# Optimization experiments

Hardware: AMD Instinct MI355X
Metric: run time of the kernel (lower is better)

## Reference

```python
import jax, jax.numpy as jnp
import numpy as np

C = 1.0      # base manifold curvature (Lorentz c)
C_E = 1.0    # expert manifold curvature (all experts init to c=1.0)
K = 1        # n_activated_experts (top-k)
SCALE = 2.0  # LResNet scale for shared-expert combine
EPS = 1e-8


def _lorentz_swiglu(x, W1, W3, W2, c_mid, c_out, prescale):
    """LorentzExpert / LorentzFeedForward: SwiGLU on space coords with Lorentz time lift.
    x: [T, D] (full Lorentz vector). W1,W3: [I-1, D]; W2: [D-1, I]. Returns [T, D]."""
    if prescale:
        x = x * np.float32(np.sqrt(C_E / C))  # x * sqrt(c_expert / c)
    s1 = jax.nn.silu(x @ W1.T)                 # [T, I-1] w1(x, return_space=True)
    s3 = x @ W3.T                              # [T, I-1] w3(x, return_space=True)
    sp = s1 * s3                               # gated space part
    t = jnp.sqrt(jnp.clip((sp * sp).sum(-1, keepdims=True) + c_mid, EPS))
    h = jnp.concatenate([t, sp], axis=-1)      # [T, I] point on expert manifold
    o = h @ W2.T                               # [T, D-1] w2 space output
    ot = jnp.sqrt(jnp.clip((o * o).sum(-1, keepdims=True) + c_out, EPS))
    return jnp.concatenate([ot, o], axis=-1)   # [T, D] on base manifold


def setup_inputs() -> dict:
    key = jax.random.key(0)
    ks = jax.random.split(key, 9)
    T, D, E, I = 2048, 1024, 8, 1024
    x = jax.random.normal(ks[0], (T, D), jnp.float32)
    gate_w = jax.random.normal(ks[1], (E, D - 1), jnp.float32) / np.sqrt(D - 1)
    gate_b = jax.random.normal(ks[2], (E,), jnp.float32) * 0.01
    W1 = jax.random.normal(ks[3], (E, I - 1, D), jnp.float32) / np.sqrt(D)
    W3 = jax.random.normal(ks[4], (E, I - 1, D), jnp.float32) / np.sqrt(D)
    W2 = jax.random.normal(ks[5], (E, D - 1, I), jnp.float32) / np.sqrt(I)
    Ws1 = jax.random.normal(ks[6], (I - 1, D), jnp.float32) / np.sqrt(D)
    Ws3 = jax.random.normal(ks[7], (I - 1, D), jnp.float32) / np.sqrt(D)
    Ws2 = jax.random.normal(ks[8], (D - 1, I), jnp.float32) / np.sqrt(I)
    return {"x": x, "gate_w": gate_w, "gate_b": gate_b, "W1": W1, "W3": W3,
            "W2": W2, "Ws1": Ws1, "Ws3": Ws3, "Ws2": Ws2}


def reference(x, gate_w, gate_b, W1, W3, W2, Ws1, Ws3, Ws2):
    T, D = x.shape
    E = gate_w.shape[0]
    # ---- Gate (softmax scoring, n_groups == 1, route_scale == 1.0) ----
    logits = x[:, 1:] @ gate_w.T                                    # [T, E]
    scores = jax.nn.softmax(logits.astype(jnp.float32), axis=-1)
    biased = scores + gate_b                                        # bias only affects routing
    _, idx = jax.lax.top_k(biased, K)                               # [T, K]
    weights = jnp.take_along_axis(scores, idx, axis=-1).astype(x.dtype)  # [T, K]
    # dense per-token expert gate weights [T, E]
    oh = jax.nn.one_hot(idx, E, dtype=x.dtype)                      # [T, K, E]
    gw = (oh * weights[..., None]).sum(axis=1)                      # [T, E]
    # ---- y init: project(zeros) -> [sqrt(c), 0, ..., 0] ----
    y0 = jnp.concatenate([jnp.full((T, 1), np.sqrt(C), x.dtype),
                          jnp.zeros((T, D - 1), x.dtype)], axis=-1)
    # ---- routed experts (dense reference: every expert on every token, masked combine) ----
    e_out = jax.vmap(lambda w1, w3, w2: _lorentz_swiglu(x, w1, w3, w2, C_E, C, True))(W1, W3, W2)  # [E, T, D]
    y = y0 + jnp.einsum('te,etd->td', gw, e_out)
    # ---- shared expert (LorentzFeedForward, stays on base manifold) ----
    z = _lorentz_swiglu(x, Ws1, Ws3, Ws2, C, C, False)
    # ---- LResNet weighted sum: normalize (z + scale*y) back to manifold ----
    comb = z + SCALE * y
    li = (comb[:, 1:] ** 2).sum(-1, keepdims=True) - comb[:, :1] ** 2  # Lorentz inner <comb,comb>
    out = np.float32(np.sqrt(C)) * comb / jnp.sqrt(jnp.clip(jnp.abs(li), EPS))
    return out
```

## Files before the change

### kernel.cpp

```cpp
#include <hip/hip_runtime.h>

typedef __bf16 bf16;
typedef __attribute__((ext_vector_type(8))) __bf16 bf16x8;
typedef __attribute__((ext_vector_type(4))) float floatx4;

#define TOK 2048
#define DD  1024
#define NE  8
#define SMAX 24

#define MFMA16(A,B,C) __builtin_amdgcn_mfma_f32_16x16x32_bf16(A,B,C,0,0,0)

__device__ __forceinline__ void load_lds16(const bf16* g, bf16* l) {
  __builtin_amdgcn_global_load_lds(
      (const __attribute__((address_space(1))) void*)g,
      (__attribute__((address_space(3))) void*)l, 16, 0, 0);
}

#define WBAR(N) asm volatile("s_waitcnt vmcnt(" #N ")\n\ts_barrier" ::: "memory")
#define BARO    asm volatile("s_barrier" ::: "memory")

#define NCVT (8*2046 + 2046 + 8*1023 + 1023)
#define GATEB TOK
__global__ __launch_bounds__(256) void prep_kernel(
    const float* __restrict__ x, const float* __restrict__ gate_w,
    const float* __restrict__ gate_b,
    const float* __restrict__ W1, const float* __restrict__ W3,
    const float* __restrict__ W2, const float* __restrict__ Ws1,
    const float* __restrict__ Ws3, const float* __restrict__ Ws2,
    bf16* __restrict__ x_bf, int* __restrict__ eidx, float* __restrict__ ewgt,
    float* __restrict__ ss,
    bf16* __restrict__ w13, bf16* __restrict__ ws13,
    bf16* __restrict__ w2b, bf16* __restrict__ ws2b,
    float* __restrict__ w2c0_r, float* __restrict__ w2c0_s,
    bf16* __restrict__ h_r, bf16* __restrict__ h_s)
{
  const int bid = blockIdx.x, tid = threadIdx.x;

  if (bid >= GATEB) {
    const int r = bid - GATEB;
    const float* src; bf16* dst;
    float* c0dst = nullptr;
    if (r < 8 * 2046) {
      const int e = r / 2046, q = r % 2046;
      src = ((q & 1) ? W3 : W1) + ((size_t)e * 1023 + (q >> 1)) * 1024;
      dst = w13 + (size_t)r * 1024;
    } else if (r < 8 * 2046 + 2046) {
      const int q = r - 8 * 2046;
      src = ((q & 1) ? Ws3 : Ws1) + (size_t)(q >> 1) * 1024;
      dst = ws13 + (size_t)q * 1024;
    } else if (r < 8 * 2046 + 2046 + 8 * 1023) {
      const int q = r - (8 * 2046 + 2046);
      src = W2 + (size_t)q * 1024;
      dst = w2b + (size_t)q * 1024;
      c0dst = w2c0_r + (size_t)(q / 1023) * 1024 + (q % 1023);
    } else {
      const int q = r - (8 * 2046 + 2046 + 8 * 1023);
      src = Ws2 + (size_t)q * 1024;
      dst = ws2b + (size_t)q * 1024;
      c0dst = w2c0_s + q;
    }
    const float4 f = ((const float4*)src)[tid];
    if (tid == 0 && c0dst) *c0dst = f.x;
    union { bf16 h[4]; uint2 u; } p;
    p.h[0] = (bf16)f.x; p.h[1] = (bf16)f.y; p.h[2] = (bf16)f.z; p.h[3] = (bf16)f.w;
    ((uint2*)dst)[tid] = p.u;
    return;
  }

  const int t = bid;
  if (tid < 2) ss[tid * TOK + t] = 0.f;
  if (tid == 2) h_r[(size_t)t * 1024] = (bf16)0.f;
  if (tid == 3) h_s[(size_t)t * 1024] = (bf16)0.f;
  const float4 v = ((const float4*)(x + (size_t)t * DD))[tid];
  union { bf16 h[4]; uint2 u; } pk;
  pk.h[0] = (bf16)v.x; pk.h[1] = (bf16)v.y; pk.h[2] = (bf16)v.z; pk.h[3] = (bf16)v.w;
  ((uint2*)(x_bf + (size_t)t * DD))[tid] = pk.u;

  float acc[NE];
#pragma unroll
  for (int e = 0; e < NE; ++e) acc[e] = 0.f;
  const float vv[4] = {v.x, v.y, v.z, v.w};
#pragma unroll
  for (int i = 0; i < 4; ++i) {
    const int d = tid * 4 + i;
    if (d >= 1) {
#pragma unroll
      for (int e = 0; e < NE; ++e) acc[e] += vv[i] * gate_w[e * (DD - 1) + d - 1];
    }
  }
#pragma unroll
  for (int off = 32; off > 0; off >>= 1) {
#pragma unroll
    for (int e = 0; e < NE; ++e) acc[e] += __shfl_down(acc[e], off);
  }
  __shared__ float red[4][NE];
  const int wid = tid >> 6, lane = tid & 63;
  if (lane == 0) {
#pragma unroll
    for (int e = 0; e < NE; ++e) red[wid][e] = acc[e];
  }
  __syncthreads();
  if (tid == 0) {
    float lg[NE];
#pragma unroll
    for (int e = 0; e < NE; ++e) lg[e] = red[0][e] + red[1][e] + red[2][e] + red[3][e];
    float m = lg[0];
    for (int e = 1; e < NE; ++e) m = fmaxf(m, lg[e]);
    float ex[NE], s = 0.f;
    for (int e = 0; e < NE; ++e) { ex[e] = expf(lg[e] - m); s += ex[e]; }
    const float inv = 1.f / s;
    int best = 0; float bb = ex[0] * inv + gate_b[0];
    for (int e = 1; e < NE; ++e) {
      const float b = ex[e] * inv + gate_b[e];
      if (b > bb) { bb = b; best = e; }
    }
    eidx[t] = best;
    ewgt[t] = ex[best] * inv;
  }
}

__global__ __launch_bounds__(256) void route_kernel(
    const int* __restrict__ eidx, int* __restrict__ perm,
    int* __restrict__ pos_of, int4* __restrict__ wl, int* __restrict__ n1)
{
  __shared__ int cnt[NE], off[NE], bas[NE + 1];
  const int tid = threadIdx.x;
  if (tid < NE) cnt[tid] = 0;
  __syncthreads();
  for (int t = tid; t < TOK; t += 256) atomicAdd(&cnt[eidx[t]], 1);
  __syncthreads();
  if (tid == 0) {
    int run = 0;
    for (int e = 0; e < NE; ++e) { bas[e] = run; off[e] = run; run += cnt[e]; }
    bas[NE] = run;
    int n = 0;
    for (int e = 0; e < NE; ++e)
      for (int r0 = 0; r0 < cnt[e]; r0 += 256) {
        int rows = cnt[e] - r0; if (rows > 256) rows = 256;
        wl[n++] = make_int4(bas[e] + r0, rows, e, 0);
      }
    for (int r0 = 0; r0 < TOK; r0 += 256) wl[n++] = make_int4(r0, 256, NE, 0);
    *n1 = n;
  }
  __syncthreads();
  for (int t = tid; t < TOK; t += 256) {
    const int e = eidx[t];
    const int p = atomicAdd(&off[e], 1);
    perm[p] = t;
    pos_of[t] = p;
  }
}

__global__ __launch_bounds__(1024) void mlp1_kernel(
    const bf16* __restrict__ x_bf, const bf16* __restrict__ w13,
    const bf16* __restrict__ ws13,
    const int* __restrict__ perm, const int4* __restrict__ wl,
    const int* __restrict__ wl_n,
    bf16* __restrict__ h_r, bf16* __restrict__ h_s,
    float* __restrict__ ss_r, float* __restrict__ ss_z)
{
  const int bid = blockIdx.x;
  const int slot = bid % SMAX, nt = bid / SMAX;
  if (slot >= *wl_n) return;
  const int4 wle = wl[slot];
  const int mbase = wle.x, rows = wle.y, eid = wle.z;
  const int tid = threadIdx.x;
  const bool routed = (eid < NE);
  const bf16* bmat = routed ? w13 + (size_t)eid * 2046 * 1024 : ws13;
  bf16* hbuf  = routed ? h_r : h_s;
  float* ssbuf = routed ? ss_r : ss_z;

  extern __shared__ __align__(16) bf16 smem[];
  bf16* const Asb[2] = {smem, smem + 16384};
  bf16* const Bsb[2] = {smem + 32768, smem + 49152};
  __shared__ int toks[256];
  if (tid < 256) {
    int r = tid < rows ? tid : rows - 1;
    toks[tid] = routed ? perm[mbase + r] : (mbase + r);
  }
  __syncthreads();

  const int wid = tid >> 6, lane = tid & 63;
  const int srow = lane >> 3;
  const int kbg  = (lane & 7) ^ (srow & 7);
  const bf16 *aG0, *aG1, *bG0, *bG1;
  int aL0o, aL1o, bL0o, bL1o;
  {
    const int r0 = wid * 16;
    aG0 = x_bf + (size_t)toks[r0 + 0 + srow] * 1024 + kbg * 8;
    aG1 = x_bf + (size_t)toks[r0 + 8 + srow] * 1024 + kbg * 8;
    aL0o = (r0 + 0) * 64; aL1o = (r0 + 8) * 64;
    int b0 = nt * 256 + r0 + 0 + srow; if (b0 > 2045) b0 = 2045;
    int b1 = nt * 256 + r0 + 8 + srow; if (b1 > 2045) b1 = 2045;
    bG0 = bmat + (size_t)b0 * 1024 + kbg * 8;
    bG1 = bmat + (size_t)b1 * 1024 + kbg * 8;
    bL0o = (r0 + 0) * 64; bL1o = (r0 + 8) * 64;
  }

  const int lrow = lane & 15, quad = lane >> 4, sw = lane & 7;
  const int wrow = (wid >> 2) * 64, wcol = (wid & 3) * 64;
  int aoff[4], boff[4], koff[2];
#pragma unroll
  for (int mi = 0; mi < 4; ++mi) aoff[mi] = (wrow + mi * 16 + lrow) * 64;
#pragma unroll
  for (int ni = 0; ni < 4; ++ni) boff[ni] = (wcol + ni * 16 + lrow) * 64;
#pragma unroll
  for (int kk = 0; kk < 2; ++kk) koff[kk] = ((kk * 4 + quad) ^ sw) * 8;

  const floatx4 fz = {0.f, 0.f, 0.f, 0.f};
  floatx4 acc[4][4];
#pragma unroll
  for (int mi = 0; mi < 4; ++mi)
#pragma unroll
    for (int ni = 0; ni < 4; ++ni) acc[mi][ni] = fz;

#define STAGE1(KE, BUF) { \
    load_lds16(aG0 + (KE), Asb[BUF] + aL0o); load_lds16(aG1 + (KE), Asb[BUF] + aL1o); \
    load_lds16(bG0 + (KE), Bsb[BUF] + bL0o); load_lds16(bG1 + (KE), Bsb[BUF] + bL1o); }

#define COMP1(BUF) { \
_Pragma("unroll") \
    for (int kk = 0; kk < 2; ++kk) { \
      bf16x8 av[4], bv[4]; \
_Pragma("unroll") \
      for (int mi = 0; mi < 4; ++mi) av[mi] = *(const bf16x8*)(Asb[BUF] + aoff[mi] + koff[kk]); \
_Pragma("unroll") \
      for (int ni = 0; ni < 4; ++ni) bv[ni] = *(const bf16x8*)(Bsb[BUF] + boff[ni] + koff[kk]); \
_Pragma("unroll") \
      for (int mi = 0; mi < 4; ++mi) \
_Pragma("unroll") \
        for (int ni = 0; ni < 4; ++ni) \
          acc[mi][ni] = MFMA16(av[mi], bv[ni], acc[mi][ni]); \
    } }

  STAGE1(0, 0)
  STAGE1(64, 1)
#pragma unroll 1
  for (int t = 0; t < 7; ++t) {
    const int ke = t * 128;
    WBAR(4); COMP1(0) BARO; STAGE1(ke + 128, 0)
    WBAR(4); COMP1(1) BARO; STAGE1(ke + 192, 1)
  }
  WBAR(4); COMP1(0)
  WBAR(0); COMP1(1)
#undef STAGE1
#undef COMP1

#pragma unroll
  for (int mi = 0; mi < 4; ++mi) {
#pragma unroll
    for (int r = 0; r < 4; ++r) {
      const int row = wrow + mi * 16 + quad * 4 + r;
      const bool rowok = row < rows;
      float ssum = 0.f;
#pragma unroll
      for (int ni = 0; ni < 4; ++ni) {
        const float c = acc[mi][ni][r];
        const float partner = __shfl_xor(c, 1);
        const float s1 = (lane & 1) ? partner : c;
        const float s3 = (lane & 1) ? c : partner;
        const float sp = (s1 / (1.f + __expf(-s1))) * s3;
        const int P = (nt * 256 + wcol + ni * 16 + lrow) >> 1;
        const bool ok = rowok && ((lane & 1) == 0) && (P < 1023);
        if (ok) hbuf[(size_t)(mbase + row) * 1024 + 1 + P] = (bf16)sp;
        ssum += ok ? sp * sp : 0.f;
      }
      ssum += __shfl_xor(ssum, 1);
      ssum += __shfl_xor(ssum, 2);
      ssum += __shfl_xor(ssum, 4);
      ssum += __shfl_xor(ssum, 8);
      if (lrow == 0 && rowok) atomicAdd(ssbuf + mbase + row, ssum);
    }
  }
}

__global__ __launch_bounds__(1024) void mlp2_kernel(
    const bf16* __restrict__ h_r, const bf16* __restrict__ h_s,
    const bf16* __restrict__ w2b, const bf16* __restrict__ ws2b,
    const int4* __restrict__ wl, const int* __restrict__ wl_n,
    float* __restrict__ o_r0, float* __restrict__ o_r1,
    float* __restrict__ o_s0, float* __restrict__ o_s1)
{
  const int bid = blockIdx.x;
  const int slot = bid % SMAX;
  const int rest = bid / SMAX;
  const int nt = rest & 3, kh = rest >> 2;
  if (slot >= *wl_n) return;
  const int4 wle = wl[slot];
  const int mbase = wle.x, rows = wle.y, eid = wle.z;
  const int tid = threadIdx.x;
  const bool routed = (eid < NE);
  const bf16* abuf = routed ? h_r : h_s;
  const bf16* bmat = routed ? w2b + (size_t)eid * 1023 * 1024 : ws2b;
  float* obuf = routed ? (kh ? o_r1 : o_r0) : (kh ? o_s1 : o_s0);
  const int n0 = nt * 256;
  const int kbase = kh * 512;

  extern __shared__ __align__(16) bf16 smem[];
  bf16* const Asb[2] = {smem, smem + 16384};
  bf16* const Bsb[2] = {smem + 32768, smem + 49152};

  const int wid = tid >> 6, lane = tid & 63;
  const int srow = lane >> 3;
  const int kbg  = (lane & 7) ^ (srow & 7);
  const bf16 *aG0, *aG1, *bG0, *bG1;
  int aL0o, aL1o, bL0o, bL1o;
  {
    const int r0 = wid * 16;
    int ra0 = r0 + 0 + srow; if (ra0 >= rows) ra0 = rows - 1;
    int ra1 = r0 + 8 + srow; if (ra1 >= rows) ra1 = rows - 1;
    aG0 = abuf + (size_t)(mbase + ra0) * 1024 + kbase + kbg * 8;
    aG1 = abuf + (size_t)(mbase + ra1) * 1024 + kbase + kbg * 8;
    aL0o = (r0 + 0) * 64; aL1o = (r0 + 8) * 64;
    int b0 = n0 + r0 + 0 + srow; if (b0 > 1022) b0 = 1022;
    int b1 = n0 + r0 + 8 + srow; if (b1 > 1022) b1 = 1022;
    bG0 = bmat + (size_t)b0 * 1024 + kbase + kbg * 8;
    bG1 = bmat + (size_t)b1 * 1024 + kbase + kbg * 8;
    bL0o = (r0 + 0) * 64; bL1o = (r0 + 8) * 64;
  }

  const int lrow = lane & 15, quad = lane >> 4, sw = lane & 7;
  const int wrow = (wid >> 2) * 64, wcol = (wid & 3) * 64;
  int aoff[4], boff[4], koff[2];
#pragma unroll
  for (int mi = 0; mi < 4; ++mi) aoff[mi] = (wrow + mi * 16 + lrow) * 64;
#pragma unroll
  for (int ni = 0; ni < 4; ++ni) boff[ni] = (wcol + ni * 16 + lrow) * 64;
#pragma unroll
  for (int kk = 0; kk < 2; ++kk) koff[kk] = ((kk * 4 + quad) ^ sw) * 8;

  const floatx4 fz = {0.f, 0.f, 0.f, 0.f};
  floatx4 acc[4][4];
#pragma unroll
  for (int mi = 0; mi < 4; ++mi)
#pragma unroll
    for (int ni = 0; ni < 4; ++ni) acc[mi][ni] = fz;

#define STAGE2(KE, BUF) { \
    load_lds16(aG0 + (KE), Asb[BUF] + aL0o); load_lds16(aG1 + (KE), Asb[BUF] + aL1o); \
    load_lds16(bG0 + (KE), Bsb[BUF] + bL0o); load_lds16(bG1 + (KE), Bsb[BUF] + bL1o); }

#define COMP2(BUF) { \
_Pragma("unroll") \
    for (int kk = 0; kk < 2; ++kk) { \
      bf16x8 av[4], bv[4]; \
_Pragma("unroll") \
      for (int mi = 0; mi < 4; ++mi) av[mi] = *(const bf16x8*)(Asb[BUF] + aoff[mi] + koff[kk]); \
_Pragma("unroll") \
      for (int ni = 0; ni < 4; ++ni) bv[ni] = *(const bf16x8*)(Bsb[BUF] + boff[ni] + koff[kk]); \
_Pragma("unroll") \
      for (int mi = 0; mi < 4; ++mi) \
_Pragma("unroll") \
        for (int ni = 0; ni < 4; ++ni) \
          acc[mi][ni] = MFMA16(av[mi], bv[ni], acc[mi][ni]); \
    } }

  STAGE2(0, 0)
  STAGE2(64, 1)
#pragma unroll 1
  for (int t = 0; t < 3; ++t) {
    const int ke = t * 128;
    WBAR(4); COMP2(0) BARO; STAGE2(ke + 128, 0)
    WBAR(4); COMP2(1) BARO; STAGE2(ke + 192, 1)
  }
  WBAR(4); COMP2(0)
  WBAR(0); COMP2(1)
#undef STAGE2
#undef COMP2

#pragma unroll
  for (int mi = 0; mi < 4; ++mi) {
#pragma unroll
    for (int r = 0; r < 4; ++r) {
      const int row = wrow + mi * 16 + quad * 4 + r;
      if (row < rows) {
        float* orow = obuf + (size_t)(mbase + row) * 1024;
#pragma unroll
        for (int ni = 0; ni < 4; ++ni) {
          const int n = n0 + wcol + ni * 16 + lrow;
          if (n < 1023) orow[n] = acc[mi][ni][r];
        }
      }
    }
  }
}

__global__ __launch_bounds__(256) void combine_kernel(
    const float* __restrict__ o_r0, const float* __restrict__ o_r1,
    const float* __restrict__ o_s0, const float* __restrict__ o_s1,
    const float* __restrict__ ss_r, const float* __restrict__ ss_z,
    const float* __restrict__ w2c0_r, const float* __restrict__ w2c0_s,
    const int* __restrict__ eidx, const int* __restrict__ pos_of,
    const float* __restrict__ wgt, float* __restrict__ out)
{
  const int t = blockIdx.x, tid = threadIdx.x;
  const int p = pos_of[t];
  const int e = eidx[t];
  const float w = wgt[t];
  const float tz = sqrtf(ss_z[t] + 1.f);
  const float tr = sqrtf(ss_r[p] + 1.f);
  const float4 oz0 = ((const float4*)(o_s0 + (size_t)t * 1024))[tid];
  const float4 oz1 = ((const float4*)(o_s1 + (size_t)t * 1024))[tid];
  const float4 oe0 = ((const float4*)(o_r0 + (size_t)p * 1024))[tid];
  const float4 oe1 = ((const float4*)(o_r1 + (size_t)p * 1024))[tid];
  const float4 c0s = ((const float4*)(w2c0_s))[tid];
  const float4 c0r = ((const float4*)(w2c0_r + (size_t)e * 1024))[tid];
  const bool last = (tid == 255);
  float ozf0 = oz0.x + oz1.x + tz * c0s.x;
  float ozf1 = oz0.y + oz1.y + tz * c0s.y;
  float ozf2 = oz0.z + oz1.z + tz * c0s.z;
  float ozf3 = last ? 0.f : (oz0.w + oz1.w + tz * c0s.w);
  float oef0 = oe0.x + oe1.x + tr * c0r.x;
  float oef1 = oe0.y + oe1.y + tr * c0r.y;
  float oef2 = oe0.z + oe1.z + tr * c0r.z;
  float oef3 = last ? 0.f : (oe0.w + oe1.w + tr * c0r.w);
  const float tw = 2.f * w;
  const float c0 = ozf0 + tw * oef0;
  const float c1 = ozf1 + tw * oef1;
  const float c2 = ozf2 + tw * oef2;
  const float c3 = ozf3 + tw * oef3;
  float sc = c0 * c0 + c1 * c1 + c2 * c2 + c3 * c3;
  float sz = ozf0 * ozf0 + ozf1 * ozf1 + ozf2 * ozf2 + ozf3 * ozf3;
  float sr = oef0 * oef0 + oef1 * oef1 + oef2 * oef2 + oef3 * oef3;
#pragma unroll
  for (int off = 32; off > 0; off >>= 1) {
    sc += __shfl_down(sc, off);
    sz += __shfl_down(sz, off);
    sr += __shfl_down(sr, off);
  }
  __shared__ float rs[3][4];
  if ((tid & 63) == 0) {
    rs[0][tid >> 6] = sc; rs[1][tid >> 6] = sz; rs[2][tid >> 6] = sr;
  }
  __syncthreads();
  const float space2 = rs[0][0] + rs[0][1] + rs[0][2] + rs[0][3];
  const float ss_oz  = rs[1][0] + rs[1][1] + rs[1][2] + rs[1][3];
  const float ss_or  = rs[2][0] + rs[2][1] + rs[2][2] + rs[2][3];
  const float comb0 = sqrtf(ss_oz + 1.f) + 2.f + 2.f * w * sqrtf(ss_or + 1.f);
  const float li = space2 - comb0 * comb0;
  const float inv = 1.f / sqrtf(fmaxf(fabsf(li), 1e-8f));
  float* orow = out + (size_t)t * 1024;
  const int j = 1 + tid * 4;
  orow[j]     = c0 * inv;
  orow[j + 1] = c1 * inv;
  orow[j + 2] = c2 * inv;
  if (!last) orow[j + 3] = c3 * inv;
  if (tid == 0) orow[0] = comb0 * inv;
}

extern "C" void kernel_launch(void* const* d_in, const int* in_sizes, int n_in,
                              void* d_out, int out_size, void* d_ws, size_t ws_size,
                              hipStream_t stream) {
  const float* x      = (const float*)d_in[0];
  const float* gate_w = (const float*)d_in[1];
  const float* gate_b = (const float*)d_in[2];
  const float* W1     = (const float*)d_in[3];
  const float* W3     = (const float*)d_in[4];
  const float* W2     = (const float*)d_in[5];
  const float* Ws1    = (const float*)d_in[6];
  const float* Ws3    = (const float*)d_in[7];
  const float* Ws2    = (const float*)d_in[8];
  float* out = (float*)d_out;

  char* ws = (char*)d_ws;
  size_t off = 0;
  auto alloc = [&](size_t bytes) {
    void* p = ws + off;
    off += (bytes + 255) & ~(size_t)255;
    return p;
  };
  bf16*  x_bf = (bf16*) alloc((size_t)TOK * 1024 * 2);
  bf16*  h_r  = (bf16*) alloc((size_t)TOK * 1024 * 2);
  bf16*  h_s  = (bf16*) alloc((size_t)TOK * 1024 * 2);
  float* o_r0 = (float*)alloc((size_t)TOK * 1024 * 4);
  float* o_s0 = (float*)alloc((size_t)TOK * 1024 * 4);
  float* ss   = (float*)alloc((size_t)2 * TOK * 4);
  int*   eidx = (int*)  alloc((size_t)TOK * 4);
  float* ewgt = (float*)alloc((size_t)TOK * 4);
  int*   perm = (int*)  alloc((size_t)TOK * 4);
  int*   posf = (int*)  alloc((size_t)TOK * 4);
  int4*  wl1  = (int4*) alloc((size_t)SMAX * 16);
  int*   wn   = (int*)  alloc(32);
  float* w2c0_r = (float*)alloc((size_t)NE * 1024 * 4);
  float* w2c0_s = (float*)alloc((size_t)1024 * 4);
  bf16*  w13  = (bf16*) alloc((size_t)8 * 2046 * 1024 * 2);
  bf16*  ws13 = (bf16*) alloc((size_t)2046 * 1024 * 2);
  bf16*  w2b  = (bf16*) alloc((size_t)8 * 1023 * 1024 * 2);
  bf16*  ws2b = (bf16*) alloc((size_t)1023 * 1024 * 2);

  float* o_r1 = (float*)w13;
  float* o_s1 = (float*)w13 + (size_t)TOK * 1024;

  float* ss_r  = ss;
  float* ss_z  = ss + TOK;

  const int MLP_LDS = 2 * (256 * 64 + 256 * 64) * 2;
  (void)hipFuncSetAttribute((const void*)mlp1_kernel,
                            hipFuncAttributeMaxDynamicSharedMemorySize, MLP_LDS);
  (void)hipFuncSetAttribute((const void*)mlp2_kernel,
                            hipFuncAttributeMaxDynamicSharedMemorySize, MLP_LDS);

  prep_kernel<<<GATEB + NCVT, 256, 0, stream>>>(
      x, gate_w, gate_b, W1, W3, W2, Ws1, Ws3, Ws2,
      x_bf, eidx, ewgt, ss, w13, ws13, w2b, ws2b, w2c0_r, w2c0_s, h_r, h_s);
  route_kernel<<<1, 256, 0, stream>>>(eidx, perm, posf, wl1, wn);
  mlp1_kernel<<<8 * SMAX, 1024, MLP_LDS, stream>>>(x_bf, w13, ws13, perm, wl1, wn,
                                                   h_r, h_s, ss_r, ss_z);
  mlp2_kernel<<<8 * SMAX, 1024, MLP_LDS, stream>>>(h_r, h_s, w2b, ws2b, wl1, wn,
                                                   o_r0, o_r1, o_s0, o_s1);
  combine_kernel<<<TOK, 256, 0, stream>>>(o_r0, o_r1, o_s0, o_s1, ss_r, ss_z,
                                          w2c0_r, w2c0_s, eidx, posf, ewgt, out);
}
```

Baseline: 231.6 us.

## Fuse routing into prep and combine into mlp2 via atomic completion counters

Folds the routing step into the prep kernel: the last gate block to finish, detected with a global atomic counter, builds the permutation and worklist. It also folds the combine step into mlp2: each token's counter is bumped by every tile that produces a piece of its output, and the block that brings it to 16 (2 routed plus 2 shared tiles per column tile) does the Lorentz normalization. The weight conversion is also widened to 8 elements per thread with half as many blocks. This removes two kernel launches and the route kernel's serial gap, in exchange for atomic traffic, threadfences and a combine tail that runs serially per token inside mlp2 blocks. Correctness depends on memory ordering across blocks, and the counters are never zeroed, relying on modulo wraparound across calls.

```diff
diff --git a/kernel.cpp b/kernel.cpp
--- a/kernel.cpp
+++ b/kernel.cpp
@@ -20,7 +20,15 @@
 #define WBAR(N) asm volatile("s_waitcnt vmcnt(" #N ")\n\ts_barrier" ::: "memory")
 #define BARO    asm volatile("s_barrier" ::: "memory")
 
+__device__ __forceinline__ uint4 pack_bf8(float4 a, float4 b) {
+  union { bf16 h[8]; uint4 u; } p;
+  p.h[0] = (bf16)a.x; p.h[1] = (bf16)a.y; p.h[2] = (bf16)a.z; p.h[3] = (bf16)a.w;
+  p.h[4] = (bf16)b.x; p.h[5] = (bf16)b.y; p.h[6] = (bf16)b.z; p.h[7] = (bf16)b.w;
+  return p.u;
+}
+
 #define NCVT (8*2046 + 2046 + 8*1023 + 1023)
+#define NCVT2 ((NCVT + 1) / 2)
 #define GATEB TOK
 __global__ __launch_bounds__(256) void prep_kernel(
     const float* __restrict__ x, const float* __restrict__ gate_w,
@@ -33,38 +41,44 @@
     bf16* __restrict__ w13, bf16* __restrict__ ws13,
     bf16* __restrict__ w2b, bf16* __restrict__ ws2b,
     float* __restrict__ w2c0_r, float* __restrict__ w2c0_s,
-    bf16* __restrict__ h_r, bf16* __restrict__ h_s)
+    bf16* __restrict__ h_r, bf16* __restrict__ h_s,
+    unsigned* __restrict__ done,
+    int* __restrict__ perm, int* __restrict__ pos_of,
+    int4* __restrict__ wl, int* __restrict__ wl_n)
 {
   const int bid = blockIdx.x, tid = threadIdx.x;
 
   if (bid >= GATEB) {
-    const int r = bid - GATEB;
-    const float* src; bf16* dst;
-    float* c0dst = nullptr;
-    if (r < 8 * 2046) {
-      const int e = r / 2046, q = r % 2046;
-      src = ((q & 1) ? W3 : W1) + ((size_t)e * 1023 + (q >> 1)) * 1024;
-      dst = w13 + (size_t)r * 1024;
-    } else if (r < 8 * 2046 + 2046) {
-      const int q = r - 8 * 2046;
-      src = ((q & 1) ? Ws3 : Ws1) + (size_t)(q >> 1) * 1024;
-      dst = ws13 + (size_t)q * 1024;
-    } else if (r < 8 * 2046 + 2046 + 8 * 1023) {
-      const int q = r - (8 * 2046 + 2046);
-      src = W2 + (size_t)q * 1024;
-      dst = w2b + (size_t)q * 1024;
-      c0dst = w2c0_r + (size_t)(q / 1023) * 1024 + (q % 1023);
-    } else {
-      const int q = r - (8 * 2046 + 2046 + 8 * 1023);
-      src = Ws2 + (size_t)q * 1024;
-      dst = ws2b + (size_t)q * 1024;
-      c0dst = w2c0_s + q;
-    }
-    const float4 f = ((const float4*)src)[tid];
-    if (tid == 0 && c0dst) *c0dst = f.x;
-    union { bf16 h[4]; uint2 u; } p;
-    p.h[0] = (bf16)f.x; p.h[1] = (bf16)f.y; p.h[2] = (bf16)f.z; p.h[3] = (bf16)f.w;
-    ((uint2*)dst)[tid] = p.u;
+    const int j = bid - GATEB;
+    const int r = j * 2 + (tid >> 7);
+    if (r < NCVT) {
+      const int tid2 = tid & 127;
+      const float* src; bf16* dst;
+      float* c0dst = nullptr;
+      if (r < 8 * 2046) {
+        const int e = r / 2046, q = r % 2046;
+        src = ((q & 1) ? W3 : W1) + ((size_t)e * 1023 + (q >> 1)) * 1024;
+        dst = w13 + (size_t)r * 1024;
+      } else if (r < 8 * 2046 + 2046) {
+        const int q = r - 8 * 2046;
+        src = ((q & 1) ? Ws3 : Ws1) + (size_t)(q >> 1) * 1024;
+        dst = ws13 + (size_t)q * 1024;
+      } else if (r < 8 * 2046 + 2046 + 8 * 1023) {
+        const int q = r - (8 * 2046 + 2046);
+        src = W2 + (size_t)q * 1024;
+        dst = w2b + (size_t)q * 1024;
+        c0dst = w2c0_r + (size_t)(q / 1023) * 1024 + (q % 1023);
+      } else {
+        const int q = r - (8 * 2046 + 2046 + 8 * 1023);
+        src = Ws2 + (size_t)q * 1024;
+        dst = ws2b + (size_t)q * 1024;
+        c0dst = w2c0_s + q;
+      }
+      const float4 f0 = ((const float4*)src)[tid2 * 2];
+      const float4 f1 = ((const float4*)src)[tid2 * 2 + 1];
+      if (tid2 == 0 && c0dst) *c0dst = f0.x;
+      ((uint4*)dst)[tid2] = pack_bf8(f0, f1);
+    }
     return;
   }
 
@@ -95,6 +109,7 @@
     for (int e = 0; e < NE; ++e) acc[e] += __shfl_down(acc[e], off);
   }
   __shared__ float red[4][NE];
+  __shared__ int iswin;
   const int wid = tid >> 6, lane = tid & 63;
   if (lane == 0) {
 #pragma unroll
@@ -117,18 +132,18 @@
     }
     eidx[t] = best;
     ewgt[t] = ex[best] * inv;
-  }
-}
-
-__global__ __launch_bounds__(256) void route_kernel(
-    const int* __restrict__ eidx, int* __restrict__ perm,
-    int* __restrict__ pos_of, int4* __restrict__ wl, int* __restrict__ n1)
-{
+    __threadfence();
+    const unsigned old = atomicAdd(done, 1u);
+    iswin = ((old & (unsigned)(GATEB - 1)) == (unsigned)(GATEB - 1)) ? 1 : 0;
+  }
+  __syncthreads();
+  if (!iswin) return;
+
+  __threadfence();
   __shared__ int cnt[NE], off[NE], bas[NE + 1];
-  const int tid = threadIdx.x;
   if (tid < NE) cnt[tid] = 0;
   __syncthreads();
-  for (int t = tid; t < TOK; t += 256) atomicAdd(&cnt[eidx[t]], 1);
+  for (int tt = tid; tt < TOK; tt += 256) atomicAdd(&cnt[eidx[tt]], 1);
   __syncthreads();
   if (tid == 0) {
     int run = 0;
@@ -141,14 +156,14 @@
         wl[n++] = make_int4(bas[e] + r0, rows, e, 0);
       }
     for (int r0 = 0; r0 < TOK; r0 += 256) wl[n++] = make_int4(r0, 256, NE, 0);
-    *n1 = n;
-  }
-  __syncthreads();
-  for (int t = tid; t < TOK; t += 256) {
-    const int e = eidx[t];
+    *wl_n = n;
+  }
+  __syncthreads();
+  for (int tt = tid; tt < TOK; tt += 256) {
+    const int e = eidx[tt];
     const int p = atomicAdd(&off[e], 1);
-    perm[p] = t;
-    pos_of[t] = p;
+    perm[p] = tt;
+    pos_of[tt] = p;
   }
 }
 
@@ -279,8 +294,14 @@
     const bf16* __restrict__ h_r, const bf16* __restrict__ h_s,
     const bf16* __restrict__ w2b, const bf16* __restrict__ ws2b,
     const int4* __restrict__ wl, const int* __restrict__ wl_n,
+    const int* __restrict__ perm,
     float* __restrict__ o_r0, float* __restrict__ o_r1,
-    float* __restrict__ o_s0, float* __restrict__ o_s1)
+    float* __restrict__ o_s0, float* __restrict__ o_s1,
+    const float* __restrict__ ss_r, const float* __restrict__ ss_z,
+    const float* __restrict__ w2c0_r, const float* __restrict__ w2c0_s,
+    const int* __restrict__ eidx, const int* __restrict__ pos_of,
+    const float* __restrict__ wgt,
+    unsigned* __restrict__ tokcnt, float* __restrict__ out)
 {
   const int bid = blockIdx.x;
   const int slot = bid % SMAX;
@@ -384,69 +405,86 @@
       }
     }
   }
-}
-
-__global__ __launch_bounds__(256) void combine_kernel(
-    const float* __restrict__ o_r0, const float* __restrict__ o_r1,
-    const float* __restrict__ o_s0, const float* __restrict__ o_s1,
-    const float* __restrict__ ss_r, const float* __restrict__ ss_z,
-    const float* __restrict__ w2c0_r, const float* __restrict__ w2c0_s,
-    const int* __restrict__ eidx, const int* __restrict__ pos_of,
-    const float* __restrict__ wgt, float* __restrict__ out)
-{
-  const int t = blockIdx.x, tid = threadIdx.x;
-  const int p = pos_of[t];
-  const int e = eidx[t];
-  const float w = wgt[t];
-  const float tz = sqrtf(ss_z[t] + 1.f);
-  const float tr = sqrtf(ss_r[p] + 1.f);
-  const float4 oz0 = ((const float4*)(o_s0 + (size_t)t * 1024))[tid];
-  const float4 oz1 = ((const float4*)(o_s1 + (size_t)t * 1024))[tid];
-  const float4 oe0 = ((const float4*)(o_r0 + (size_t)p * 1024))[tid];
-  const float4 oe1 = ((const float4*)(o_r1 + (size_t)p * 1024))[tid];
-  const float4 c0s = ((const float4*)(w2c0_s))[tid];
-  const float4 c0r = ((const float4*)(w2c0_r + (size_t)e * 1024))[tid];
-  const bool last = (tid == 255);
-  float ozf0 = oz0.x + oz1.x + tz * c0s.x;
-  float ozf1 = oz0.y + oz1.y + tz * c0s.y;
-  float ozf2 = oz0.z + oz1.z + tz * c0s.z;
-  float ozf3 = last ? 0.f : (oz0.w + oz1.w + tz * c0s.w);
-  float oef0 = oe0.x + oe1.x + tr * c0r.x;
-  float oef1 = oe0.y + oe1.y + tr * c0r.y;
-  float oef2 = oe0.z + oe1.z + tr * c0r.z;
-  float oef3 = last ? 0.f : (oe0.w + oe1.w + tr * c0r.w);
-  const float tw = 2.f * w;
-  const float c0 = ozf0 + tw * oef0;
-  const float c1 = ozf1 + tw * oef1;
-  const float c2 = ozf2 + tw * oef2;
-  const float c3 = ozf3 + tw * oef3;
-  float sc = c0 * c0 + c1 * c1 + c2 * c2 + c3 * c3;
-  float sz = ozf0 * ozf0 + ozf1 * ozf1 + ozf2 * ozf2 + ozf3 * ozf3;
-  float sr = oef0 * oef0 + oef1 * oef1 + oef2 * oef2 + oef3 * oef3;
-#pragma unroll
-  for (int off = 32; off > 0; off >>= 1) {
-    sc += __shfl_down(sc, off);
-    sz += __shfl_down(sz, off);
-    sr += __shfl_down(sr, off);
-  }
+
+  __shared__ int wtok[256];
+  __shared__ int wcnt;
   __shared__ float rs[3][4];
-  if ((tid & 63) == 0) {
-    rs[0][tid >> 6] = sc; rs[1][tid >> 6] = sz; rs[2][tid >> 6] = sr;
-  }
-  __syncthreads();
-  const float space2 = rs[0][0] + rs[0][1] + rs[0][2] + rs[0][3];
-  const float ss_oz  = rs[1][0] + rs[1][1] + rs[1][2] + rs[1][3];
-  const float ss_or  = rs[2][0] + rs[2][1] + rs[2][2] + rs[2][3];
-  const float comb0 = sqrtf(ss_oz + 1.f) + 2.f + 2.f * w * sqrtf(ss_or + 1.f);
-  const float li = space2 - comb0 * comb0;
-  const float inv = 1.f / sqrtf(fmaxf(fabsf(li), 1e-8f));
-  float* orow = out + (size_t)t * 1024;
-  const int j = 1 + tid * 4;
-  orow[j]     = c0 * inv;
-  orow[j + 1] = c1 * inv;
-  orow[j + 2] = c2 * inv;
-  if (!last) orow[j + 3] = c3 * inv;
-  if (tid == 0) orow[0] = comb0 * inv;
+  if (tid == 0) wcnt = 0;
+  __syncthreads();
+  __threadfence();
+  if (tid < rows) {
+    const int t = routed ? perm[mbase + tid] : (mbase + tid);
+    const unsigned old = atomicAdd(&tokcnt[t], 1u);
+    if ((old & 15u) == 15u) {
+      const int i = atomicAdd(&wcnt, 1);
+      wtok[i] = t;
+    }
+  }
+  __syncthreads();
+  const int nw = wcnt;
+  if (nw == 0) return;
+  __threadfence();
+
+  for (int i = 0; i < nw; ++i) {
+    const int t = wtok[i];
+    float c0 = 0.f, c1 = 0.f, c2 = 0.f, c3 = 0.f;
+    float sc = 0.f, sz = 0.f, sr = 0.f;
+    if (tid < 256) {
+      const int p = pos_of[t];
+      const int e = eidx[t];
+      const float w = wgt[t];
+      const float tz = sqrtf(ss_z[t] + 1.f);
+      const float tr = sqrtf(ss_r[p] + 1.f);
+      const float4 oz0 = ((const float4*)(o_s0 + (size_t)t * 1024))[tid];
+      const float4 oz1 = ((const float4*)(o_s1 + (size_t)t * 1024))[tid];
+      const float4 oe0 = ((const float4*)(o_r0 + (size_t)p * 1024))[tid];
+      const float4 oe1 = ((const float4*)(o_r1 + (size_t)p * 1024))[tid];
+      const float4 c0s = ((const float4*)(w2c0_s))[tid];
+      const float4 c0r = ((const float4*)(w2c0_r + (size_t)e * 1024))[tid];
+      const bool last = (tid == 255);
+      const float ozf0 = oz0.x + oz1.x + tz * c0s.x;
+      const float ozf1 = oz0.y + oz1.y + tz * c0s.y;
+      const float ozf2 = oz0.z + oz1.z + tz * c0s.z;
+      const float ozf3 = last ? 0.f : (oz0.w + oz1.w + tz * c0s.w);
+      const float oef0 = oe0.x + oe1.x + tr * c0r.x;
+      const float oef1 = oe0.y + oe1.y + tr * c0r.y;
+      const float oef2 = oe0.z + oe1.z + tr * c0r.z;
+      const float oef3 = last ? 0.f : (oe0.w + oe1.w + tr * c0r.w);
+      const float tw = 2.f * w;
+      c0 = ozf0 + tw * oef0;
+      c1 = ozf1 + tw * oef1;
+      c2 = ozf2 + tw * oef2;
+      c3 = ozf3 + tw * oef3;
+      sc = c0 * c0 + c1 * c1 + c2 * c2 + c3 * c3;
+      sz = ozf0 * ozf0 + ozf1 * ozf1 + ozf2 * ozf2 + ozf3 * ozf3;
+      sr = oef0 * oef0 + oef1 * oef1 + oef2 * oef2 + oef3 * oef3;
+#pragma unroll
+      for (int off = 32; off > 0; off >>= 1) {
+        sc += __shfl_down(sc, off);
+        sz += __shfl_down(sz, off);
+        sr += __shfl_down(sr, off);
+      }
+      if (lane == 0) { rs[0][wid] = sc; rs[1][wid] = sz; rs[2][wid] = sr; }
+    }
+    __syncthreads();
+    if (tid < 256) {
+      const float space2 = rs[0][0] + rs[0][1] + rs[0][2] + rs[0][3];
+      const float ss_oz  = rs[1][0] + rs[1][1] + rs[1][2] + rs[1][3];
+      const float ss_or  = rs[2][0] + rs[2][1] + rs[2][2] + rs[2][3];
+      const float w = wgt[t];
+      const float comb0 = sqrtf(ss_oz + 1.f) + 2.f + 2.f * w * sqrtf(ss_or + 1.f);
+      const float li = space2 - comb0 * comb0;
+      const float inv = 1.f / sqrtf(fmaxf(fabsf(li), 1e-8f));
+      float* orow = out + (size_t)t * 1024;
+      const int j = 1 + tid * 4;
+      orow[j]     = c0 * inv;
+      orow[j + 1] = c1 * inv;
+      orow[j + 2] = c2 * inv;
+      if (tid != 255) orow[j + 3] = c3 * inv;
+      if (tid == 0) orow[0] = comb0 * inv;
+    }
+    __syncthreads();
+  }
 }
 
 extern "C" void kernel_launch(void* const* d_in, const int* in_sizes, int n_in,
@@ -482,6 +520,8 @@
   int*   posf = (int*)  alloc((size_t)TOK * 4);
   int4*  wl1  = (int4*) alloc((size_t)SMAX * 16);
   int*   wn   = (int*)  alloc(32);
+  unsigned* done   = (unsigned*)alloc(32);
+  unsigned* tokcnt = (unsigned*)alloc((size_t)TOK * 4);
   float* w2c0_r = (float*)alloc((size_t)NE * 1024 * 4);
   float* w2c0_s = (float*)alloc((size_t)1024 * 4);
   bf16*  w13  = (bf16*) alloc((size_t)8 * 2046 * 1024 * 2);
@@ -501,14 +541,14 @@
   (void)hipFuncSetAttribute((const void*)mlp2_kernel,
                             hipFuncAttributeMaxDynamicSharedMemorySize, MLP_LDS);
 
-  prep_kernel<<<GATEB + NCVT, 256, 0, stream>>>(
+  prep_kernel<<<GATEB + NCVT2, 256, 0, stream>>>(
       x, gate_w, gate_b, W1, W3, W2, Ws1, Ws3, Ws2,
-      x_bf, eidx, ewgt, ss, w13, ws13, w2b, ws2b, w2c0_r, w2c0_s, h_r, h_s);
-  route_kernel<<<1, 256, 0, stream>>>(eidx, perm, posf, wl1, wn);
+      x_bf, eidx, ewgt, ss, w13, ws13, w2b, ws2b, w2c0_r, w2c0_s, h_r, h_s,
+      done, perm, posf, wl1, wn);
   mlp1_kernel<<<8 * SMAX, 1024, MLP_LDS, stream>>>(x_bf, w13, ws13, perm, wl1, wn,
                                                    h_r, h_s, ss_r, ss_z);
-  mlp2_kernel<<<8 * SMAX, 1024, MLP_LDS, stream>>>(h_r, h_s, w2b, ws2b, wl1, wn,
-                                                   o_r0, o_r1, o_s0, o_s1);
-  combine_kernel<<<TOK, 256, 0, stream>>>(o_r0, o_r1, o_s0, o_s1, ss_r, ss_z,
-                                          w2c0_r, w2c0_s, eidx, posf, ewgt, out);
+  mlp2_kernel<<<8 * SMAX, 1024, MLP_LDS, stream>>>(h_r, h_s, w2b, ws2b, wl1, wn, perm,
+                                                   o_r0, o_r1, o_s0, o_s1,
+                                                   ss_r, ss_z, w2c0_r, w2c0_s,
+                                                   eidx, posf, ewgt, tokcnt, out);
 }
```

Result: slower. 720.5 us (+211.2%).

## Fuse combine into mlp2 via grid-wide atomic barrier

Applied to the files above, without the earlier changes.

Merges the combine kernel into the mlp2 GEMM kernel. All 192 blocks count into a global atomic, spin until every block has finished its GEMM tile, and then each block runs the per-token Lorentz normalization for four tokens per round over three rounds. The aim is to drop one kernel launch and its tail gap. In exchange the combine phase runs on only 192 blocks instead of 2048. The barrier also assumes every block is co-resident at once (1024 threads and 128KB LDS each), which risks deadlock if the GPU cannot hold them all.

```diff
diff --git a/kernel.cpp b/kernel.cpp
--- a/kernel.cpp
+++ b/kernel.cpp
@@ -8,6 +8,7 @@
 #define DD  1024
 #define NE  8
 #define SMAX 24
+#define GRID2 (8 * SMAX)
 
 #define MFMA16(A,B,C) __builtin_amdgcn_mfma_f32_16x16x32_bf16(A,B,C,0,0,0)
 
@@ -122,10 +123,12 @@
 
 __global__ __launch_bounds__(256) void route_kernel(
     const int* __restrict__ eidx, int* __restrict__ perm,
-    int* __restrict__ pos_of, int4* __restrict__ wl, int* __restrict__ n1)
+    int* __restrict__ pos_of, int4* __restrict__ wl, int* __restrict__ n1,
+    unsigned* __restrict__ done2)
 {
   __shared__ int cnt[NE], off[NE], bas[NE + 1];
   const int tid = threadIdx.x;
+  if (tid == 0) *done2 = 0u;
   if (tid < NE) cnt[tid] = 0;
   __syncthreads();
   for (int t = tid; t < TOK; t += 256) atomicAdd(&cnt[eidx[t]], 1);
@@ -280,62 +283,69 @@
     const bf16* __restrict__ w2b, const bf16* __restrict__ ws2b,
     const int4* __restrict__ wl, const int* __restrict__ wl_n,
     float* __restrict__ o_r0, float* __restrict__ o_r1,
-    float* __restrict__ o_s0, float* __restrict__ o_s1)
+    float* __restrict__ o_s0, float* __restrict__ o_s1,
+    const float* __restrict__ ss_r, const float* __restrict__ ss_z,
+    const float* __restrict__ w2c0_r, const float* __restrict__ w2c0_s,
+    const int* __restrict__ eidx, const int* __restrict__ pos_of,
+    const float* __restrict__ wgt,
+    unsigned* __restrict__ done2, float* __restrict__ out)
 {
   const int bid = blockIdx.x;
   const int slot = bid % SMAX;
   const int rest = bid / SMAX;
   const int nt = rest & 3, kh = rest >> 2;
-  if (slot >= *wl_n) return;
-  const int4 wle = wl[slot];
-  const int mbase = wle.x, rows = wle.y, eid = wle.z;
   const int tid = threadIdx.x;
-  const bool routed = (eid < NE);
-  const bf16* abuf = routed ? h_r : h_s;
-  const bf16* bmat = routed ? w2b + (size_t)eid * 1023 * 1024 : ws2b;
-  float* obuf = routed ? (kh ? o_r1 : o_r0) : (kh ? o_s1 : o_s0);
-  const int n0 = nt * 256;
-  const int kbase = kh * 512;
-
+  const int wid = tid >> 6, lane = tid & 63;
   extern __shared__ __align__(16) bf16 smem[];
-  bf16* const Asb[2] = {smem, smem + 16384};
-  bf16* const Bsb[2] = {smem + 32768, smem + 49152};
-
-  const int wid = tid >> 6, lane = tid & 63;
-  const int srow = lane >> 3;
-  const int kbg  = (lane & 7) ^ (srow & 7);
-  const bf16 *aG0, *aG1, *bG0, *bG1;
-  int aL0o, aL1o, bL0o, bL1o;
-  {
-    const int r0 = wid * 16;
-    int ra0 = r0 + 0 + srow; if (ra0 >= rows) ra0 = rows - 1;
-    int ra1 = r0 + 8 + srow; if (ra1 >= rows) ra1 = rows - 1;
-    aG0 = abuf + (size_t)(mbase + ra0) * 1024 + kbase + kbg * 8;
-    aG1 = abuf + (size_t)(mbase + ra1) * 1024 + kbase + kbg * 8;
-    aL0o = (r0 + 0) * 64; aL1o = (r0 + 8) * 64;
-    int b0 = n0 + r0 + 0 + srow; if (b0 > 1022) b0 = 1022;
-    int b1 = n0 + r0 + 8 + srow; if (b1 > 1022) b1 = 1022;
-    bG0 = bmat + (size_t)b0 * 1024 + kbase + kbg * 8;
-    bG1 = bmat + (size_t)b1 * 1024 + kbase + kbg * 8;
-    bL0o = (r0 + 0) * 64; bL1o = (r0 + 8) * 64;
-  }
-
-  const int lrow = lane & 15, quad = lane >> 4, sw = lane & 7;
-  const int wrow = (wid >> 2) * 64, wcol = (wid & 3) * 64;
-  int aoff[4], boff[4], koff[2];
-#pragma unroll
-  for (int mi = 0; mi < 4; ++mi) aoff[mi] = (wrow + mi * 16 + lrow) * 64;
-#pragma unroll
-  for (int ni = 0; ni < 4; ++ni) boff[ni] = (wcol + ni * 16 + lrow) * 64;
-#pragma unroll
-  for (int kk = 0; kk < 2; ++kk) koff[kk] = ((kk * 4 + quad) ^ sw) * 8;
-
-  const floatx4 fz = {0.f, 0.f, 0.f, 0.f};
-  floatx4 acc[4][4];
-#pragma unroll
-  for (int mi = 0; mi < 4; ++mi)
-#pragma unroll
-    for (int ni = 0; ni < 4; ++ni) acc[mi][ni] = fz;
+  const bool active = (slot < *wl_n);
+
+  if (active) {
+    const int4 wle = wl[slot];
+    const int mbase = wle.x, rows = wle.y, eid = wle.z;
+    const bool routed = (eid < NE);
+    const bf16* abuf = routed ? h_r : h_s;
+    const bf16* bmat = routed ? w2b + (size_t)eid * 1023 * 1024 : ws2b;
+    float* obuf = routed ? (kh ? o_r1 : o_r0) : (kh ? o_s1 : o_s0);
+    const int n0 = nt * 256;
+    const int kbase = kh * 512;
+
+    bf16* const Asb[2] = {smem, smem + 16384};
+    bf16* const Bsb[2] = {smem + 32768, smem + 49152};
+
+    const int srow = lane >> 3;
+    const int kbg  = (lane & 7) ^ (srow & 7);
+    const bf16 *aG0, *aG1, *bG0, *bG1;
+    int aL0o, aL1o, bL0o, bL1o;
+    {
+      const int r0 = wid * 16;
+      int ra0 = r0 + 0 + srow; if (ra0 >= rows) ra0 = rows - 1;
+      int ra1 = r0 + 8 + srow; if (ra1 >= rows) ra1 = rows - 1;
+      aG0 = abuf + (size_t)(mbase + ra0) * 1024 + kbase + kbg * 8;
+      aG1 = abuf + (size_t)(mbase + ra1) * 1024 + kbase + kbg * 8;
+      aL0o = (r0 + 0) * 64; aL1o = (r0 + 8) * 64;
+      int b0 = n0 + r0 + 0 + srow; if (b0 > 1022) b0 = 1022;
+      int b1 = n0 + r0 + 8 + srow; if (b1 > 1022) b1 = 1022;
+      bG0 = bmat + (size_t)b0 * 1024 + kbase + kbg * 8;
+      bG1 = bmat + (size_t)b1 * 1024 + kbase + kbg * 8;
+      bL0o = (r0 + 0) * 64; bL1o = (r0 + 8) * 64;
+    }
+
+    const int lrow = lane & 15, quad = lane >> 4, sw = lane & 7;
+    const int wrow = (wid >> 2) * 64, wcol = (wid & 3) * 64;
+    int aoff[4], boff[4], koff[2];
+#pragma unroll
+    for (int mi = 0; mi < 4; ++mi) aoff[mi] = (wrow + mi * 16 + lrow) * 64;
+#pragma unroll
+    for (int ni = 0; ni < 4; ++ni) boff[ni] = (wcol + ni * 16 + lrow) * 64;
+#pragma unroll
+    for (int kk = 0; kk < 2; ++kk) koff[kk] = ((kk * 4 + quad) ^ sw) * 8;
+
+    const floatx4 fz = {0.f, 0.f, 0.f, 0.f};
+    floatx4 acc[4][4];
+#pragma unroll
+    for (int mi = 0; mi < 4; ++mi)
+#pragma unroll
+      for (int ni = 0; ni < 4; ++ni) acc[mi][ni] = fz;
 
 #define STAGE2(KE, BUF) { \
     load_lds16(aG0 + (KE), Asb[BUF] + aL0o); load_lds16(aG1 + (KE), Asb[BUF] + aL1o); \
@@ -356,97 +366,113 @@
           acc[mi][ni] = MFMA16(av[mi], bv[ni], acc[mi][ni]); \
     } }
 
-  STAGE2(0, 0)
-  STAGE2(64, 1)
+    STAGE2(0, 0)
+    STAGE2(64, 1)
 #pragma unroll 1
-  for (int t = 0; t < 3; ++t) {
-    const int ke = t * 128;
-    WBAR(4); COMP2(0) BARO; STAGE2(ke + 128, 0)
-    WBAR(4); COMP2(1) BARO; STAGE2(ke + 192, 1)
-  }
-  WBAR(4); COMP2(0)
-  WBAR(0); COMP2(1)
+    for (int t = 0; t < 3; ++t) {
+      const int ke = t * 128;
+      WBAR(4); COMP2(0) BARO; STAGE2(ke + 128, 0)
+      WBAR(4); COMP2(1) BARO; STAGE2(ke + 192, 1)
+    }
+    WBAR(4); COMP2(0)
+    WBAR(0); COMP2(1)
 #undef STAGE2
 #undef COMP2
 
 #pragma unroll
-  for (int mi = 0; mi < 4; ++mi) {
-#pragma unroll
-    for (int r = 0; r < 4; ++r) {
-      const int row = wrow + mi * 16 + quad * 4 + r;
-      if (row < rows) {
-        float* orow = obuf + (size_t)(mbase + row) * 1024;
-#pragma unroll
-        for (int ni = 0; ni < 4; ++ni) {
-          const int n = n0 + wcol + ni * 16 + lrow;
-          if (n < 1023) orow[n] = acc[mi][ni][r];
+    for (int mi = 0; mi < 4; ++mi) {
+#pragma unroll
+      for (int r = 0; r < 4; ++r) {
+        const int row = wrow + mi * 16 + quad * 4 + r;
+        if (row < rows) {
+          float* orow = obuf + (size_t)(mbase + row) * 1024;
+#pragma unroll
+          for (int ni = 0; ni < 4; ++ni) {
+            const int n = n0 + wcol + ni * 16 + lrow;
+            if (n < 1023) orow[n] = acc[mi][ni][r];
+          }
         }
       }
     }
   }
-}
-
-__global__ __launch_bounds__(256) void combine_kernel(
-    const float* __restrict__ o_r0, const float* __restrict__ o_r1,
-    const float* __restrict__ o_s0, const float* __restrict__ o_s1,
-    const float* __restrict__ ss_r, const float* __restrict__ ss_z,
-    const float* __restrict__ w2c0_r, const float* __restrict__ w2c0_s,
-    const int* __restrict__ eidx, const int* __restrict__ pos_of,
-    const float* __restrict__ wgt, float* __restrict__ out)
-{
-  const int t = blockIdx.x, tid = threadIdx.x;
-  const int p = pos_of[t];
-  const int e = eidx[t];
-  const float w = wgt[t];
-  const float tz = sqrtf(ss_z[t] + 1.f);
-  const float tr = sqrtf(ss_r[p] + 1.f);
-  const float4 oz0 = ((const float4*)(o_s0 + (size_t)t * 1024))[tid];
-  const float4 oz1 = ((const float4*)(o_s1 + (size_t)t * 1024))[tid];
-  const float4 oe0 = ((const float4*)(o_r0 + (size_t)p * 1024))[tid];
-  const float4 oe1 = ((const float4*)(o_r1 + (size_t)p * 1024))[tid];
-  const float4 c0s = ((const float4*)(w2c0_s))[tid];
-  const float4 c0r = ((const float4*)(w2c0_r + (size_t)e * 1024))[tid];
-  const bool last = (tid == 255);
-  float ozf0 = oz0.x + oz1.x + tz * c0s.x;
-  float ozf1 = oz0.y + oz1.y + tz * c0s.y;
-  float ozf2 = oz0.z + oz1.z + tz * c0s.z;
-  float ozf3 = last ? 0.f : (oz0.w + oz1.w + tz * c0s.w);
-  float oef0 = oe0.x + oe1.x + tr * c0r.x;
-  float oef1 = oe0.y + oe1.y + tr * c0r.y;
-  float oef2 = oe0.z + oe1.z + tr * c0r.z;
-  float oef3 = last ? 0.f : (oe0.w + oe1.w + tr * c0r.w);
-  const float tw = 2.f * w;
-  const float c0 = ozf0 + tw * oef0;
-  const float c1 = ozf1 + tw * oef1;
-  const float c2 = ozf2 + tw * oef2;
-  const float c3 = ozf3 + tw * oef3;
-  float sc = c0 * c0 + c1 * c1 + c2 * c2 + c3 * c3;
-  float sz = ozf0 * ozf0 + ozf1 * ozf1 + ozf2 * ozf2 + ozf3 * ozf3;
-  float sr = oef0 * oef0 + oef1 * oef1 + oef2 * oef2 + oef3 * oef3;
-#pragma unroll
-  for (int off = 32; off > 0; off >>= 1) {
-    sc += __shfl_down(sc, off);
-    sz += __shfl_down(sz, off);
-    sr += __shfl_down(sr, off);
-  }
-  __shared__ float rs[3][4];
-  if ((tid & 63) == 0) {
-    rs[0][tid >> 6] = sc; rs[1][tid >> 6] = sz; rs[2][tid >> 6] = sr;
-  }
-  __syncthreads();
-  const float space2 = rs[0][0] + rs[0][1] + rs[0][2] + rs[0][3];
-  const float ss_oz  = rs[1][0] + rs[1][1] + rs[1][2] + rs[1][3];
-  const float ss_or  = rs[2][0] + rs[2][1] + rs[2][2] + rs[2][3];
-  const float comb0 = sqrtf(ss_oz + 1.f) + 2.f + 2.f * w * sqrtf(ss_or + 1.f);
-  const float li = space2 - comb0 * comb0;
-  const float inv = 1.f / sqrtf(fmaxf(fabsf(li), 1e-8f));
-  float* orow = out + (size_t)t * 1024;
-  const int j = 1 + tid * 4;
-  orow[j]     = c0 * inv;
-  orow[j + 1] = c1 * inv;
-  orow[j + 2] = c2 * inv;
-  if (!last) orow[j + 3] = c3 * inv;
-  if (tid == 0) orow[0] = comb0 * inv;
+
+  __syncthreads();
+  if (tid == 0) {
+    __threadfence();
+    const unsigned m = atomicAdd(done2, 1u);
+    const unsigned tgt = (m / (unsigned)GRID2 + 1u) * (unsigned)GRID2;
+    while (atomicOr(done2, 0u) < tgt)
+      __builtin_amdgcn_s_sleep(32);
+    __threadfence();
+  }
+  __syncthreads();
+
+  __shared__ float rs2[4][3][4];
+  const int grp = tid >> 8;
+  const int q   = tid & 255;
+  const int gw  = (tid >> 6) & 3;
+  const int eng = bid * 4 + grp;
+#pragma unroll 1
+  for (int rnd = 0; rnd < 3; ++rnd) {
+    const int t = eng + rnd * 768;
+    const bool valid = t < TOK;
+    float c0 = 0.f, c1 = 0.f, c2 = 0.f, c3 = 0.f;
+    float wv = 0.f;
+    if (valid) {
+      const int p = pos_of[t];
+      const int e = eidx[t];
+      wv = wgt[t];
+      const float tz = sqrtf(ss_z[t] + 1.f);
+      const float tr = sqrtf(ss_r[p] + 1.f);
+      const float4 oz0 = ((const float4*)(o_s0 + (size_t)t * 1024))[q];
+      const float4 oz1 = ((const float4*)(o_s1 + (size_t)t * 1024))[q];
+      const float4 oe0 = ((const float4*)(o_r0 + (size_t)p * 1024))[q];
+      const float4 oe1 = ((const float4*)(o_r1 + (size_t)p * 1024))[q];
+      const float4 c0s = ((const float4*)(w2c0_s))[q];
+      const float4 c0r = ((const float4*)(w2c0_r + (size_t)e * 1024))[q];
+      const bool last = (q == 255);
+      const float ozf0 = oz0.x + oz1.x + tz * c0s.x;
+      const float ozf1 = oz0.y + oz1.y + tz * c0s.y;
+      const float ozf2 = oz0.z + oz1.z + tz * c0s.z;
+      const float ozf3 = last ? 0.f : (oz0.w + oz1.w + tz * c0s.w);
+      const float oef0 = oe0.x + oe1.x + tr * c0r.x;
+      const float oef1 = oe0.y + oe1.y + tr * c0r.y;
+      const float oef2 = oe0.z + oe1.z + tr * c0r.z;
+      const float oef3 = last ? 0.f : (oe0.w + oe1.w + tr * c0r.w);
+      const float tw = 2.f * wv;
+      c0 = ozf0 + tw * oef0;
+      c1 = ozf1 + tw * oef1;
+      c2 = ozf2 + tw * oef2;
+      c3 = ozf3 + tw * oef3;
+      float sc = c0 * c0 + c1 * c1 + c2 * c2 + c3 * c3;
+      float sz = ozf0 * ozf0 + ozf1 * ozf1 + ozf2 * ozf2 + ozf3 * ozf3;
+      float sr = oef0 * oef0 + oef1 * oef1 + oef2 * oef2 + oef3 * oef3;
+#pragma unroll
+      for (int off = 32; off > 0; off >>= 1) {
+        sc += __shfl_down(sc, off);
+        sz += __shfl_down(sz, off);
+        sr += __shfl_down(sr, off);
+      }
+      if (lane == 0) { rs2[grp][0][gw] = sc; rs2[grp][1][gw] = sz; rs2[grp][2][gw] = sr; }
+    }
+    __syncthreads();
+    if (valid) {
+      const float space2 = rs2[grp][0][0] + rs2[grp][0][1] + rs2[grp][0][2] + rs2[grp][0][3];
+      const float ss_oz  = rs2[grp][1][0] + rs2[grp][1][1] + rs2[grp][1][2] + rs2[grp][1][3];
+      const float ss_or  = rs2[grp][2][0] + rs2[grp][2][1] + rs2[grp][2][2] + rs2[grp][2][3];
+      const float comb0 = sqrtf(ss_oz + 1.f) + 2.f + 2.f * wv * sqrtf(ss_or + 1.f);
+      const float li = space2 - comb0 * comb0;
+      const float inv = 1.f / sqrtf(fmaxf(fabsf(li), 1e-8f));
+      float* orow = out + (size_t)t * 1024;
+      const int j = 1 + q * 4;
+      orow[j]     = c0 * inv;
+      orow[j + 1] = c1 * inv;
+      orow[j + 2] = c2 * inv;
+      if (q != 255) orow[j + 3] = c3 * inv;
+      if (q == 0) orow[0] = comb0 * inv;
+    }
+    __syncthreads();
+  }
 }
 
 extern "C" void kernel_launch(void* const* d_in, const int* in_sizes, int n_in,
@@ -482,6 +508,7 @@
   int*   posf = (int*)  alloc((size_t)TOK * 4);
   int4*  wl1  = (int4*) alloc((size_t)SMAX * 16);
   int*   wn   = (int*)  alloc(32);
+  unsigned* done2 = (unsigned*)alloc(32);
   float* w2c0_r = (float*)alloc((size_t)NE * 1024 * 4);
   float* w2c0_s = (float*)alloc((size_t)1024 * 4);
   bf16*  w13  = (bf16*) alloc((size_t)8 * 2046 * 1024 * 2);
@@ -504,11 +531,11 @@
   prep_kernel<<<GATEB + NCVT, 256, 0, stream>>>(
       x, gate_w, gate_b, W1, W3, W2, Ws1, Ws3, Ws2,
       x_bf, eidx, ewgt, ss, w13, ws13, w2b, ws2b, w2c0_r, w2c0_s, h_r, h_s);
-  route_kernel<<<1, 256, 0, stream>>>(eidx, perm, posf, wl1, wn);
+  route_kernel<<<1, 256, 0, stream>>>(eidx, perm, posf, wl1, wn, done2);
   mlp1_kernel<<<8 * SMAX, 1024, MLP_LDS, stream>>>(x_bf, w13, ws13, perm, wl1, wn,
                                                    h_r, h_s, ss_r, ss_z);
-  mlp2_kernel<<<8 * SMAX, 1024, MLP_LDS, stream>>>(h_r, h_s, w2b, ws2b, wl1, wn,
-                                                   o_r0, o_r1, o_s0, o_s1);
-  combine_kernel<<<TOK, 256, 0, stream>>>(o_r0, o_r1, o_s0, o_s1, ss_r, ss_z,
-                                          w2c0_r, w2c0_s, eidx, posf, ewgt, out);
+  mlp2_kernel<<<GRID2, 1024, MLP_LDS, stream>>>(h_r, h_s, w2b, ws2b, wl1, wn,
+                                                o_r0, o_r1, o_s0, o_s1,
+                                                ss_r, ss_z, w2c0_r, w2c0_s,
+                                                eidx, posf, ewgt, done2, out);
 }
```

New measurement: 250.9 us. 1.08x slower.
